# Kernel tuning notes

Measured on AMD Instinct MI355X. Metric: run time of the kernel, lower is better.

## Reference

```python
import jax, jax.numpy as jnp
import numpy as np
import math

H = 768      # hidden_dim
NH = 12      # nhead
HD = H // NH # head_dim
FF = 4 * H
B, N = 8, 1024


def _layernorm(x, g, b, eps=1e-5):
    m = jnp.mean(x, axis=-1, keepdims=True)
    v = jnp.var(x, axis=-1, keepdims=True)
    return (x - m) * jax.lax.rsqrt(v + eps) * g + b


def setup_inputs() -> dict:
    key = jax.random.key(0)
    ks = jax.random.split(key, 16)
    s = 1.0 / math.sqrt(H)
    inp = {
        'x': jax.random.normal(ks[0], (B, N, H), jnp.float32),
        'attn_bias': jax.random.normal(ks[1], (NH, N, N), jnp.float32),
        'Wq': jax.random.normal(ks[2], (H, H), jnp.float32) * s,
        'bq': jnp.zeros((H,), jnp.float32),
        'Wk': jax.random.normal(ks[3], (H, H), jnp.float32) * s,
        'bk': jnp.zeros((H,), jnp.float32),
        'Wv': jax.random.normal(ks[4], (H, H), jnp.float32) * s,
        'bv': jnp.zeros((H,), jnp.float32),
        'Wo': jax.random.normal(ks[5], (H, H), jnp.float32) * s,
        'bo': jnp.zeros((H,), jnp.float32),
        'g1': jnp.ones((H,), jnp.float32),
        'be1': jnp.zeros((H,), jnp.float32),
        'W1': jax.random.normal(ks[6], (H, FF), jnp.float32) * s,
        'bf1': jnp.zeros((FF,), jnp.float32),
        'W2': jax.random.normal(ks[7], (FF, H), jnp.float32) * (1.0 / math.sqrt(FF)),
        'bf2': jnp.zeros((H,), jnp.float32),
        'g2': jnp.ones((H,), jnp.float32),
        'be2': jnp.zeros((H,), jnp.float32),
    }
    return inp


def reference(x, attn_bias, Wq, bq, Wk, bk, Wv, bv, Wo, bo, g1, be1, W1, bf1, W2, bf2, g2, be2):
    # dropout in eval mode (identity)
    Bc, Nc, C = x.shape
    q = (x @ Wq + bq).reshape(Bc, Nc, NH, HD).transpose(0, 2, 1, 3)  # [B,H,N,D]
    k = (x @ Wk + bk).reshape(Bc, Nc, NH, HD).transpose(0, 2, 1, 3)
    v = (x @ Wv + bv).reshape(Bc, Nc, NH, HD).transpose(0, 2, 1, 3)
    scores = jnp.einsum('bhnd,bhmd->bhnm', q, k) / math.sqrt(HD)
    scores = scores + attn_bias[None]  # bias broadcast over batch
    probs = jax.nn.softmax(scores, axis=-1)
    out = jnp.einsum('bhnm,bhmd->bhnd', probs, v)
    out = out.transpose(0, 2, 1, 3).reshape(Bc, Nc, C)
    out = out @ Wo + bo
    x = _layernorm(x + out, g1, be1)
    h = jax.nn.gelu(x @ W1 + bf1, approximate=False) @ W2 + bf2
    x = _layernorm(x + h, g2, be2)
    return x
```

## Files before the change

### kernel.cpp

```cpp
#include <hip/hip_runtime.h>
#include <math.h>

#define NH 12
#define HD 64
#define SEQ 1024
#define BATCH 8
#define HDIM 768
#define FFDIM 3072
#define MTOT (BATCH*SEQ)

typedef __attribute__((ext_vector_type(8))) short short8;
typedef __attribute__((ext_vector_type(4))) float f32x4;
typedef __attribute__((ext_vector_type(4))) unsigned short ushort4v;

__device__ __forceinline__ unsigned short f2b(float f) {
    union { float f; unsigned u; } v; v.f = f;
    unsigned r = v.u + 0x7fffu + ((v.u >> 16) & 1u);
    return (unsigned short)(r >> 16);
}

__device__ __forceinline__ f32x4 mfma16(short8 a, short8 b, f32x4 c) {
    return __builtin_amdgcn_mfma_f32_16x16x32_bf16(a, b, c, 0, 0, 0);
}

__global__ __launch_bounds__(256) void k_cvt(const float* __restrict__ in,
                                             unsigned short* __restrict__ out, int n) {
    int idx = (blockIdx.x * 256 + threadIdx.x) * 4;
    if (idx >= n) return;
    float4 v = *reinterpret_cast<const float4*>(in + idx);
    ushort4v o;
    o[0] = f2b(v.x); o[1] = f2b(v.y); o[2] = f2b(v.z); o[3] = f2b(v.w);
    *reinterpret_cast<ushort4v*>(out + idx) = o;
}

__global__ __launch_bounds__(256) void k_wt(const float* __restrict__ W,
                                            unsigned short* __restrict__ WT, int K, int Nn) {
    __shared__ float t[32][33];
    int n0 = blockIdx.x * 32, k0 = blockIdx.y * 32;
    int x = threadIdx.x, y = threadIdx.y;
#pragma unroll
    for (int i = y; i < 32; i += 8) t[i][x] = W[(size_t)(k0 + i) * Nn + n0 + x];
    __syncthreads();
#pragma unroll
    for (int i = y; i < 32; i += 8) WT[(size_t)(n0 + i) * K + k0 + x] = f2b(t[x][i]);
}

__global__ void k_bias3(const float* __restrict__ a, const float* __restrict__ b,
                        const float* __restrict__ c, float* __restrict__ o) {
    int i = blockIdx.x * 256 + threadIdx.x;
    if (i >= 3 * HDIM) return;
    o[i] = (i < HDIM) ? a[i] : (i < 2 * HDIM ? b[i - HDIM] : c[i - 2 * HDIM]);
}

template<int EPI>
__global__ __launch_bounds__(256) void k_gemm(const unsigned short* __restrict__ A,
                                              const unsigned short* __restrict__ BT,
                                              const float* __restrict__ bias,
                                              const float* __restrict__ resid,
                                              unsigned short* __restrict__ outb,
                                              float* __restrict__ outf,
                                              int Mdim, int Ndim, int Kdim) {
    __shared__ unsigned short As[128][40];
    __shared__ unsigned short Bs[128][40];
    int tid = threadIdx.x;
    int wid = tid >> 6, lane = tid & 63;
    int wm = wid >> 1, wn = wid & 1;
    int l15 = lane & 15, l16 = lane >> 4;
    int bm = blockIdx.x * 128, bn = blockIdx.y * 128;

    f32x4 acc[4][4] = {};

    for (int kt = 0; kt < Kdim; kt += 32) {
#pragma unroll
        for (int it = 0; it < 2; ++it) {
            int idx = tid + it * 256;
            int r = idx >> 2, c8 = (idx & 3) * 8;
            *reinterpret_cast<short8*>(&As[r][c8]) =
                *reinterpret_cast<const short8*>(&A[(size_t)(bm + r) * Kdim + kt + c8]);
            *reinterpret_cast<short8*>(&Bs[r][c8]) =
                *reinterpret_cast<const short8*>(&BT[(size_t)(bn + r) * Kdim + kt + c8]);
        }
        __syncthreads();
        short8 af[4], bfr[4];
#pragma unroll
        for (int i = 0; i < 4; i++)
            af[i] = *reinterpret_cast<const short8*>(&As[wm * 64 + i * 16 + l15][l16 * 8]);
#pragma unroll
        for (int i = 0; i < 4; i++)
            bfr[i] = *reinterpret_cast<const short8*>(&Bs[wn * 64 + i * 16 + l15][l16 * 8]);
#pragma unroll
        for (int i = 0; i < 4; i++)
#pragma unroll
            for (int j = 0; j < 4; j++)
                acc[i][j] = mfma16(af[i], bfr[j], acc[i][j]);
        __syncthreads();
    }

#pragma unroll
    for (int i = 0; i < 4; i++) {
#pragma unroll
        for (int j = 0; j < 4; j++) {
            int grow0 = bm + wm * 64 + i * 16 + l16 * 4;
            int gcol = bn + wn * 64 + j * 16 + l15;
            float bcol = bias[gcol];
#pragma unroll
            for (int r = 0; r < 4; r++) {
                int grow = grow0 + r;
                float v = acc[i][j][r] + bcol;
                size_t oi = (size_t)grow * Ndim + gcol;
                if constexpr (EPI == 0) {
                    outb[oi] = f2b(v);
                } else if constexpr (EPI == 1) {
                    outf[oi] = v + resid[oi];
                } else {
                    float g = 0.5f * v * (1.0f + erff(v * 0.70710678118654752f));
                    outb[oi] = f2b(g);
                }
            }
        }
    }
}

__global__ __launch_bounds__(256) void k_attn(const unsigned short* __restrict__ QKV,
                                              const float* __restrict__ bias,
                                              unsigned short* __restrict__ out) {
    __shared__ unsigned short Ks[64][72];
    __shared__ unsigned short Vt[64][72];
    __shared__ unsigned short Ps[4][16][72];

    int bh = blockIdx.y;
    int b = bh / NH, h = bh % NH;
    int q0 = blockIdx.x * 64;
    int tid = threadIdx.x, wid = tid >> 6, lane = tid & 63;
    int l15 = lane & 15, l16 = lane >> 4;

    size_t qrow = (size_t)(b * SEQ + q0 + wid * 16 + l15) * 2304 + h * 64;
    short8 qf0 = *reinterpret_cast<const short8*>(&QKV[qrow + l16 * 8]);
    short8 qf1 = *reinterpret_cast<const short8*>(&QKV[qrow + 32 + l16 * 8]);

    f32x4 o[4] = {};
    float mrow[4], lrow[4];
#pragma unroll
    for (int r = 0; r < 4; r++) { mrow[r] = -1e30f; lrow[r] = 0.0f; }

    for (int kt = 0; kt < SEQ; kt += 64) {
#pragma unroll
        for (int it = 0; it < 2; ++it) {
            int idx = tid + it * 256;
            int r = idx >> 3, c8 = (idx & 7) * 8;
            size_t gr = (size_t)(b * SEQ + kt + r) * 2304 + h * 64;
            *reinterpret_cast<short8*>(&Ks[r][c8]) =
                *reinterpret_cast<const short8*>(&QKV[gr + 768 + c8]);
            short8 vv = *reinterpret_cast<const short8*>(&QKV[gr + 1536 + c8]);
            int cc = r ^ c8;
#pragma unroll
            for (int j = 0; j < 8; j++) Vt[c8 + j][cc] = (unsigned short)vv[j];
        }
        __syncthreads();

        f32x4 s[4];
#pragma unroll
        for (int c = 0; c < 4; c++) {
            f32x4 t = {};
            t = mfma16(qf0, *reinterpret_cast<const short8*>(&Ks[c * 16 + l15][l16 * 8]), t);
            t = mfma16(qf1, *reinterpret_cast<const short8*>(&Ks[c * 16 + l15][32 + l16 * 8]), t);
            s[c] = t;
        }
#pragma unroll
        for (int c = 0; c < 4; c++)
#pragma unroll
            for (int r = 0; r < 4; r++) {
                size_t bi = (size_t)h * SEQ * SEQ +
                            (size_t)(q0 + wid * 16 + l16 * 4 + r) * SEQ + kt + c * 16 + l15;
                s[c][r] = s[c][r] * 0.125f + bias[bi];
            }
#pragma unroll
        for (int r = 0; r < 4; r++) {
            float mx = fmaxf(fmaxf(s[0][r], s[1][r]), fmaxf(s[2][r], s[3][r]));
#pragma unroll
            for (int off = 1; off < 16; off <<= 1) mx = fmaxf(mx, __shfl_xor(mx, off, 64));
            float mnew = fmaxf(mrow[r], mx);
            float resc = __expf(mrow[r] - mnew);
            mrow[r] = mnew;
            float sum = 0.0f;
#pragma unroll
            for (int c = 0; c < 4; c++) {
                float p = __expf(s[c][r] - mnew);
                s[c][r] = p; sum += p;
            }
#pragma unroll
            for (int off = 1; off < 16; off <<= 1) sum += __shfl_xor(sum, off, 64);
            lrow[r] = lrow[r] * resc + sum;
#pragma unroll
            for (int dc = 0; dc < 4; dc++) o[dc][r] *= resc;
        }
#pragma unroll
        for (int c = 0; c < 4; c++)
#pragma unroll
            for (int r = 0; r < 4; r++)
                Ps[wid][l16 * 4 + r][c * 16 + l15] = f2b(s[c][r]);
#pragma unroll
        for (int dc = 0; dc < 4; dc++) {
            int d = dc * 16 + l15;
            int sw = ((d >> 3) & 7) << 3;
#pragma unroll
            for (int kk = 0; kk < 2; kk++) {
                short8 pa = *reinterpret_cast<const short8*>(&Ps[wid][l15][kk * 32 + l16 * 8]);
                short8 vb = *reinterpret_cast<const short8*>(&Vt[d][(kk * 32 + l16 * 8) ^ sw]);
                o[dc] = mfma16(pa, vb, o[dc]);
            }
        }
        __syncthreads();
    }

#pragma unroll
    for (int dc = 0; dc < 4; dc++)
#pragma unroll
        for (int r = 0; r < 4; r++) {
            float v = o[dc][r] / lrow[r];
            size_t row = (size_t)(b * SEQ + q0 + wid * 16 + l16 * 4 + r);
            out[row * 768 + h * 64 + dc * 16 + l15] = f2b(v);
        }
}

template<int WB>
__global__ __launch_bounds__(256) void k_ln(const float* __restrict__ in,
                                            const float* __restrict__ gw,
                                            const float* __restrict__ bw,
                                            float* __restrict__ outf,
                                            unsigned short* __restrict__ outb) {
    int row = blockIdx.x, tid = threadIdx.x;
    const float* x = in + (size_t)row * 768;
    float v0 = x[tid], v1 = x[tid + 256], v2 = x[tid + 512];
    float s = v0 + v1 + v2;
    float s2 = v0 * v0 + v1 * v1 + v2 * v2;
#pragma unroll
    for (int off = 32; off; off >>= 1) {
        s += __shfl_down(s, off, 64);
        s2 += __shfl_down(s2, off, 64);
    }
    __shared__ float red[16];
    if ((tid & 63) == 0) { red[tid >> 6] = s; red[8 + (tid >> 6)] = s2; }
    __syncthreads();
    float ssum = red[0] + red[1] + red[2] + red[3];
    float s2sum = red[8] + red[9] + red[10] + red[11];
    float mean = ssum * (1.0f / 768.0f);
    float var = s2sum * (1.0f / 768.0f) - mean * mean;
    float rstd = rsqrtf(var + 1e-5f);
    float* of = outf + (size_t)row * 768;
    unsigned short* ob = outb ? outb + (size_t)row * 768 : nullptr;
    float vv[3] = { v0, v1, v2 };
#pragma unroll
    for (int i = 0; i < 3; i++) {
        int col = tid + i * 256;
        float y = (vv[i] - mean) * rstd * gw[col] + bw[col];
        of[col] = y;
        if constexpr (WB) ob[col] = f2b(y);
    }
}

constexpr size_t OFF_XB    = 0;
constexpr size_t OFF_QKV   = OFF_XB    + 12582912;
constexpr size_t OFF_ATT   = OFF_QKV   + 37748736;
constexpr size_t OFF_WQKVT = OFF_ATT   + 12582912;
constexpr size_t OFF_WOT   = OFF_WQKVT + 3538944;
constexpr size_t OFF_W1T   = OFF_WOT   + 1179648;
constexpr size_t OFF_W2T   = OFF_W1T   + 4718592;
constexpr size_t OFF_BQKV  = OFF_W2T   + 4718592;
constexpr size_t OFF_TMP   = OFF_BQKV  + 9216;
constexpr size_t OFF_X1F   = OFF_TMP   + 25165824;
constexpr size_t OFF_X1B   = OFF_X1F   + 25165824;
constexpr size_t OFF_H     = OFF_X1B   + 12582912;

extern "C" void kernel_launch(void* const* d_in, const int* in_sizes, int n_in,
                              void* d_out, int out_size, void* d_ws, size_t ws_size,
                              hipStream_t stream) {
    const float* x    = (const float*)d_in[0];
    const float* ab   = (const float*)d_in[1];
    const float* Wq   = (const float*)d_in[2];
    const float* bq   = (const float*)d_in[3];
    const float* Wk   = (const float*)d_in[4];
    const float* bk   = (const float*)d_in[5];
    const float* Wv   = (const float*)d_in[6];
    const float* bv   = (const float*)d_in[7];
    const float* Wo   = (const float*)d_in[8];
    const float* bo   = (const float*)d_in[9];
    const float* g1   = (const float*)d_in[10];
    const float* be1  = (const float*)d_in[11];
    const float* W1   = (const float*)d_in[12];
    const float* bf1  = (const float*)d_in[13];
    const float* W2   = (const float*)d_in[14];
    const float* bf2  = (const float*)d_in[15];
    const float* g2   = (const float*)d_in[16];
    const float* be2  = (const float*)d_in[17];

    char* ws = (char*)d_ws;
    unsigned short* xb    = (unsigned short*)(ws + OFF_XB);
    unsigned short* qkv   = (unsigned short*)(ws + OFF_QKV);
    unsigned short* att   = (unsigned short*)(ws + OFF_ATT);
    unsigned short* wqkvt = (unsigned short*)(ws + OFF_WQKVT);
    unsigned short* wot   = (unsigned short*)(ws + OFF_WOT);
    unsigned short* w1t   = (unsigned short*)(ws + OFF_W1T);
    unsigned short* w2t   = (unsigned short*)(ws + OFF_W2T);
    float*          bqkv  = (float*)(ws + OFF_BQKV);
    float*          tmp   = (float*)(ws + OFF_TMP);
    float*          x1f   = (float*)(ws + OFF_X1F);
    unsigned short* x1b   = (unsigned short*)(ws + OFF_X1B);
    unsigned short* hb    = (unsigned short*)(ws + OFF_H);
    float*          out   = (float*)d_out;

    k_cvt<<<dim3(MTOT * HDIM / 1024), dim3(256), 0, stream>>>(x, xb, MTOT * HDIM);
    k_wt<<<dim3(24, 24), dim3(32, 8), 0, stream>>>(Wq, wqkvt, HDIM, HDIM);
    k_wt<<<dim3(24, 24), dim3(32, 8), 0, stream>>>(Wk, wqkvt + 768 * 768, HDIM, HDIM);
    k_wt<<<dim3(24, 24), dim3(32, 8), 0, stream>>>(Wv, wqkvt + 2 * 768 * 768, HDIM, HDIM);
    k_wt<<<dim3(24, 24), dim3(32, 8), 0, stream>>>(Wo, wot, HDIM, HDIM);
    k_wt<<<dim3(96, 24), dim3(32, 8), 0, stream>>>(W1, w1t, HDIM, FFDIM);
    k_wt<<<dim3(24, 96), dim3(32, 8), 0, stream>>>(W2, w2t, FFDIM, HDIM);
    k_bias3<<<dim3(9), dim3(256), 0, stream>>>(bq, bk, bv, bqkv);

    k_gemm<0><<<dim3(64, 18), dim3(256), 0, stream>>>(xb, wqkvt, bqkv, nullptr, qkv, nullptr,
                                                      MTOT, 3 * HDIM, HDIM);
    k_attn<<<dim3(SEQ / 64, BATCH * NH), dim3(256), 0, stream>>>(qkv, ab, att);
    k_gemm<1><<<dim3(64, 6), dim3(256), 0, stream>>>(att, wot, bo, x, nullptr, tmp,
                                                     MTOT, HDIM, HDIM);
    k_ln<1><<<dim3(MTOT), dim3(256), 0, stream>>>(tmp, g1, be1, x1f, x1b);
    k_gemm<2><<<dim3(64, 24), dim3(256), 0, stream>>>(x1b, w1t, bf1, nullptr, hb, nullptr,
                                                      MTOT, FFDIM, HDIM);
    k_gemm<1><<<dim3(64, 6), dim3(256), 0, stream>>>(hb, w2t, bf2, x1f, nullptr, tmp,
                                                     MTOT, FFDIM == FFDIM ? HDIM : HDIM, FFDIM);
    k_ln<0><<<dim3(MTOT), dim3(256), 0, stream>>>(tmp, g2, be2, out, nullptr);
}
```

Before: 514.3 us.

## Use direct global-to-LDS loads in GEMM and batch-loop attention blocks

```diff
diff --git a/kernel.cpp b/kernel.cpp
--- a/kernel.cpp
+++ b/kernel.cpp
@@ -21,6 +21,12 @@
 
 __device__ __forceinline__ f32x4 mfma16(short8 a, short8 b, f32x4 c) {
     return __builtin_amdgcn_mfma_f32_16x16x32_bf16(a, b, c, 0, 0, 0);
+}
+
+__device__ __forceinline__ void async_copy16(const unsigned short* g, unsigned short* l) {
+    __builtin_amdgcn_global_load_lds(
+        (const __attribute__((address_space(1))) unsigned int*)(const void*)g,
+        (__attribute__((address_space(3))) unsigned int*)(void*)l, 16, 0, 0);
 }
 
 __global__ __launch_bounds__(256) void k_cvt(const float* __restrict__ in,
@@ -60,26 +66,29 @@
                                               unsigned short* __restrict__ outb,
                                               float* __restrict__ outf,
                                               int Mdim, int Ndim, int Kdim) {
-    __shared__ unsigned short As[128][40];
-    __shared__ unsigned short Bs[128][40];
+    __shared__ unsigned short As[128][32];
+    __shared__ unsigned short Bs[128][32];
     int tid = threadIdx.x;
     int wid = tid >> 6, lane = tid & 63;
     int wm = wid >> 1, wn = wid & 1;
     int l15 = lane & 15, l16 = lane >> 4;
     int bm = blockIdx.x * 128, bn = blockIdx.y * 128;
 
+    int srow = wid * 16 + (lane >> 2);
+    int scol = (lane & 3) * 8;
+    const unsigned short* aptr = A + (size_t)(bm + srow) * Kdim + scol;
+    const unsigned short* bptr = BT + (size_t)(bn + srow) * Kdim + scol;
+    unsigned short* alds = &As[srow][scol];
+    unsigned short* blds = &Bs[srow][scol];
+    const size_t rstep = (size_t)64 * Kdim;
+
     f32x4 acc[4][4] = {};
 
     for (int kt = 0; kt < Kdim; kt += 32) {
-#pragma unroll
-        for (int it = 0; it < 2; ++it) {
-            int idx = tid + it * 256;
-            int r = idx >> 2, c8 = (idx & 3) * 8;
-            *reinterpret_cast<short8*>(&As[r][c8]) =
-                *reinterpret_cast<const short8*>(&A[(size_t)(bm + r) * Kdim + kt + c8]);
-            *reinterpret_cast<short8*>(&Bs[r][c8]) =
-                *reinterpret_cast<const short8*>(&BT[(size_t)(bn + r) * Kdim + kt + c8]);
-        }
+        async_copy16(aptr + kt, alds);
+        async_copy16(aptr + rstep + kt, alds + 64 * 32);
+        async_copy16(bptr + kt, blds);
+        async_copy16(bptr + rstep + kt, blds + 64 * 32);
         __syncthreads();
         short8 af[4], bfr[4];
 #pragma unroll
@@ -121,6 +130,7 @@
     }
 }
 
+#define NBATCH_PER_BLK 2
 __global__ __launch_bounds__(256) void k_attn(const unsigned short* __restrict__ QKV,
                                               const float* __restrict__ bias,
                                               unsigned short* __restrict__ out) {
@@ -128,99 +138,102 @@
     __shared__ unsigned short Vt[64][72];
     __shared__ unsigned short Ps[4][16][72];
 
-    int bh = blockIdx.y;
-    int b = bh / NH, h = bh % NH;
+    int h = blockIdx.y;
     int q0 = blockIdx.x * 64;
     int tid = threadIdx.x, wid = tid >> 6, lane = tid & 63;
     int l15 = lane & 15, l16 = lane >> 4;
 
-    size_t qrow = (size_t)(b * SEQ + q0 + wid * 16 + l15) * 2304 + h * 64;
-    short8 qf0 = *reinterpret_cast<const short8*>(&QKV[qrow + l16 * 8]);
-    short8 qf1 = *reinterpret_cast<const short8*>(&QKV[qrow + 32 + l16 * 8]);
-
-    f32x4 o[4] = {};
-    float mrow[4], lrow[4];
-#pragma unroll
-    for (int r = 0; r < 4; r++) { mrow[r] = -1e30f; lrow[r] = 0.0f; }
-
-    for (int kt = 0; kt < SEQ; kt += 64) {
-#pragma unroll
-        for (int it = 0; it < 2; ++it) {
-            int idx = tid + it * 256;
-            int r = idx >> 3, c8 = (idx & 7) * 8;
-            size_t gr = (size_t)(b * SEQ + kt + r) * 2304 + h * 64;
-            *reinterpret_cast<short8*>(&Ks[r][c8]) =
-                *reinterpret_cast<const short8*>(&QKV[gr + 768 + c8]);
-            short8 vv = *reinterpret_cast<const short8*>(&QKV[gr + 1536 + c8]);
-            int cc = r ^ c8;
-#pragma unroll
-            for (int j = 0; j < 8; j++) Vt[c8 + j][cc] = (unsigned short)vv[j];
+    const float* bbase = bias + (size_t)h * SEQ * SEQ +
+                         (size_t)(q0 + wid * 16 + l16 * 4) * SEQ + l15;
+
+    for (int bi = 0; bi < NBATCH_PER_BLK; ++bi) {
+        int b = blockIdx.z * NBATCH_PER_BLK + bi;
+
+        size_t qrow = (size_t)(b * SEQ + q0 + wid * 16 + l15) * 2304 + h * 64;
+        short8 qf0 = *reinterpret_cast<const short8*>(&QKV[qrow + l16 * 8]);
+        short8 qf1 = *reinterpret_cast<const short8*>(&QKV[qrow + 32 + l16 * 8]);
+
+        f32x4 o[4] = {};
+        float mrow[4], lrow[4];
+#pragma unroll
+        for (int r = 0; r < 4; r++) { mrow[r] = -1e30f; lrow[r] = 0.0f; }
+
+        for (int kt = 0; kt < SEQ; kt += 64) {
+#pragma unroll
+            for (int it = 0; it < 2; ++it) {
+                int idx = tid + it * 256;
+                int r = idx >> 3, c8 = (idx & 7) * 8;
+                size_t gr = (size_t)(b * SEQ + kt + r) * 2304 + h * 64;
+                *reinterpret_cast<short8*>(&Ks[r][c8]) =
+                    *reinterpret_cast<const short8*>(&QKV[gr + 768 + c8]);
+                short8 vv = *reinterpret_cast<const short8*>(&QKV[gr + 1536 + c8]);
+                int cc = r ^ c8;
+#pragma unroll
+                for (int j = 0; j < 8; j++) Vt[c8 + j][cc] = (unsigned short)vv[j];
+            }
+            __syncthreads();
+
+            f32x4 s[4];
+#pragma unroll
+            for (int c = 0; c < 4; c++) {
+                f32x4 t = {};
+                t = mfma16(qf0, *reinterpret_cast<const short8*>(&Ks[c * 16 + l15][l16 * 8]), t);
+                t = mfma16(qf1, *reinterpret_cast<const short8*>(&Ks[c * 16 + l15][32 + l16 * 8]), t);
+                s[c] = t;
+            }
+#pragma unroll
+            for (int c = 0; c < 4; c++)
+#pragma unroll
+                for (int r = 0; r < 4; r++)
+                    s[c][r] = s[c][r] * 0.125f + bbase[(size_t)r * SEQ + kt + c * 16];
+#pragma unroll
+            for (int r = 0; r < 4; r++) {
+                float mx = fmaxf(fmaxf(s[0][r], s[1][r]), fmaxf(s[2][r], s[3][r]));
+#pragma unroll
+                for (int off = 1; off < 16; off <<= 1) mx = fmaxf(mx, __shfl_xor(mx, off, 64));
+                float mnew = fmaxf(mrow[r], mx);
+                float resc = __expf(mrow[r] - mnew);
+                mrow[r] = mnew;
+                float sum = 0.0f;
+#pragma unroll
+                for (int c = 0; c < 4; c++) {
+                    float p = __expf(s[c][r] - mnew);
+                    s[c][r] = p; sum += p;
+                }
+#pragma unroll
+                for (int off = 1; off < 16; off <<= 1) sum += __shfl_xor(sum, off, 64);
+                lrow[r] = lrow[r] * resc + sum;
+#pragma unroll
+                for (int dc = 0; dc < 4; dc++) o[dc][r] *= resc;
+            }
+#pragma unroll
+            for (int c = 0; c < 4; c++)
+#pragma unroll
+                for (int r = 0; r < 4; r++)
+                    Ps[wid][l16 * 4 + r][c * 16 + l15] = f2b(s[c][r]);
+#pragma unroll
+            for (int dc = 0; dc < 4; dc++) {
+                int d = dc * 16 + l15;
+                int sw = ((d >> 3) & 7) << 3;
+#pragma unroll
+                for (int kk = 0; kk < 2; kk++) {
+                    short8 pa = *reinterpret_cast<const short8*>(&Ps[wid][l15][kk * 32 + l16 * 8]);
+                    short8 vb = *reinterpret_cast<const short8*>(&Vt[d][(kk * 32 + l16 * 8) ^ sw]);
+                    o[dc] = mfma16(pa, vb, o[dc]);
+                }
+            }
+            __syncthreads();
         }
-        __syncthreads();
-
-        f32x4 s[4];
-#pragma unroll
-        for (int c = 0; c < 4; c++) {
-            f32x4 t = {};
-            t = mfma16(qf0, *reinterpret_cast<const short8*>(&Ks[c * 16 + l15][l16 * 8]), t);
-            t = mfma16(qf1, *reinterpret_cast<const short8*>(&Ks[c * 16 + l15][32 + l16 * 8]), t);
-            s[c] = t;
-        }
-#pragma unroll
-        for (int c = 0; c < 4; c++)
+
+#pragma unroll
+        for (int dc = 0; dc < 4; dc++)
 #pragma unroll
             for (int r = 0; r < 4; r++) {
-                size_t bi = (size_t)h * SEQ * SEQ +
-                            (size_t)(q0 + wid * 16 + l16 * 4 + r) * SEQ + kt + c * 16 + l15;
-                s[c][r] = s[c][r] * 0.125f + bias[bi];
-            }
-#pragma unroll
-        for (int r = 0; r < 4; r++) {
-            float mx = fmaxf(fmaxf(s[0][r], s[1][r]), fmaxf(s[2][r], s[3][r]));
-#pragma unroll
-            for (int off = 1; off < 16; off <<= 1) mx = fmaxf(mx, __shfl_xor(mx, off, 64));
-            float mnew = fmaxf(mrow[r], mx);
-            float resc = __expf(mrow[r] - mnew);
-            mrow[r] = mnew;
-            float sum = 0.0f;
-#pragma unroll
-            for (int c = 0; c < 4; c++) {
-                float p = __expf(s[c][r] - mnew);
-                s[c][r] = p; sum += p;
-            }
-#pragma unroll
-            for (int off = 1; off < 16; off <<= 1) sum += __shfl_xor(sum, off, 64);
-            lrow[r] = lrow[r] * resc + sum;
-#pragma unroll
-            for (int dc = 0; dc < 4; dc++) o[dc][r] *= resc;
-        }
-#pragma unroll
-        for (int c = 0; c < 4; c++)
-#pragma unroll
-            for (int r = 0; r < 4; r++)
-                Ps[wid][l16 * 4 + r][c * 16 + l15] = f2b(s[c][r]);
-#pragma unroll
-        for (int dc = 0; dc < 4; dc++) {
-            int d = dc * 16 + l15;
-            int sw = ((d >> 3) & 7) << 3;
-#pragma unroll
-            for (int kk = 0; kk < 2; kk++) {
-                short8 pa = *reinterpret_cast<const short8*>(&Ps[wid][l15][kk * 32 + l16 * 8]);
-                short8 vb = *reinterpret_cast<const short8*>(&Vt[d][(kk * 32 + l16 * 8) ^ sw]);
-                o[dc] = mfma16(pa, vb, o[dc]);
-            }
-        }
-        __syncthreads();
-    }
-
-#pragma unroll
-    for (int dc = 0; dc < 4; dc++)
-#pragma unroll
-        for (int r = 0; r < 4; r++) {
-            float v = o[dc][r] / lrow[r];
-            size_t row = (size_t)(b * SEQ + q0 + wid * 16 + l16 * 4 + r);
-            out[row * 768 + h * 64 + dc * 16 + l15] = f2b(v);
-        }
+                float v = o[dc][r] / lrow[r];
+                size_t row = (size_t)(b * SEQ + q0 + wid * 16 + l16 * 4 + r);
+                out[row * 768 + h * 64 + dc * 16 + l15] = f2b(v);
+            }
+    }
 }
 
 template<int WB>
@@ -320,13 +333,13 @@
 
     k_gemm<0><<<dim3(64, 18), dim3(256), 0, stream>>>(xb, wqkvt, bqkv, nullptr, qkv, nullptr,
                                                       MTOT, 3 * HDIM, HDIM);
-    k_attn<<<dim3(SEQ / 64, BATCH * NH), dim3(256), 0, stream>>>(qkv, ab, att);
+    k_attn<<<dim3(SEQ / 64, NH, BATCH / NBATCH_PER_BLK), dim3(256), 0, stream>>>(qkv, ab, att);
     k_gemm<1><<<dim3(64, 6), dim3(256), 0, stream>>>(att, wot, bo, x, nullptr, tmp,
                                                      MTOT, HDIM, HDIM);
     k_ln<1><<<dim3(MTOT), dim3(256), 0, stream>>>(tmp, g1, be1, x1f, x1b);
     k_gemm<2><<<dim3(64, 24), dim3(256), 0, stream>>>(x1b, w1t, bf1, nullptr, hb, nullptr,
                                                       MTOT, FFDIM, HDIM);
     k_gemm<1><<<dim3(64, 6), dim3(256), 0, stream>>>(hb, w2t, bf2, x1f, nullptr, tmp,
-                                                     MTOT, FFDIM == FFDIM ? HDIM : HDIM, FFDIM);
+                                                     MTOT, HDIM, FFDIM);
     k_ln<0><<<dim3(MTOT), dim3(256), 0, stream>>>(tmp, g2, be2, out, nullptr);
 }
```

Measured after the change: 560.3 us. +8.9%, slower.
